# Performance work log

Hardware: AMD Instinct MI355X
Metric: run time of the kernel (lower is better)

Reference implementation:

```python
import jax, jax.numpy as jnp
import numpy as np

SEQ_LEN, BATCH, INPUT_SIZE, HIDDEN, OUTPUT_SIZE = 100, 2048, 128, 512, 128
DEC_STEPS = 29


def lstm_cell(x, h, c, W_ih, W_hh, b_ih, b_hh):
    # torch LSTMCell gate order: i, f, g, o
    gates = x @ W_ih.T + b_ih + h @ W_hh.T + b_hh
    i, f, g, o = jnp.split(gates, 4, axis=-1)
    i = jax.nn.sigmoid(i)
    f = jax.nn.sigmoid(f)
    g = jnp.tanh(g)
    o = jax.nn.sigmoid(o)
    c_new = f * c + i * g
    h_new = o * jnp.tanh(c_new)
    return h_new, c_new


def setup_inputs() -> dict:
    key = jax.random.key(0)
    ks = jax.random.split(key, 10)
    s = 0.05
    return {
        "input": jax.random.normal(ks[0], (SEQ_LEN, BATCH, INPUT_SIZE), jnp.float32),
        "hidden_encoder": jnp.zeros((BATCH, HIDDEN), jnp.float32),
        "hidden_decoder": jnp.zeros((BATCH, HIDDEN), jnp.float32),
        "cell_encoder": jnp.zeros((BATCH, HIDDEN), jnp.float32),
        "cell_decoder": jnp.zeros((BATCH, HIDDEN), jnp.float32),
        "W_ih_enc": jax.random.normal(ks[1], (4 * HIDDEN, INPUT_SIZE), jnp.float32) * s,
        "W_hh_enc": jax.random.normal(ks[2], (4 * HIDDEN, HIDDEN), jnp.float32) * s,
        "b_ih_enc": jax.random.normal(ks[3], (4 * HIDDEN,), jnp.float32) * s,
        "b_hh_enc": jax.random.normal(ks[4], (4 * HIDDEN,), jnp.float32) * s,
        "W_ih_dec": jax.random.normal(ks[5], (4 * HIDDEN, HIDDEN), jnp.float32) * s,
        "W_hh_dec": jax.random.normal(ks[6], (4 * HIDDEN, HIDDEN), jnp.float32) * s,
        "b_ih_dec": jax.random.normal(ks[7], (4 * HIDDEN,), jnp.float32) * s,
        "b_hh_dec": jax.random.normal(ks[8], (4 * HIDDEN,), jnp.float32) * s,
        "W_lin": jax.random.normal(ks[9], (OUTPUT_SIZE, HIDDEN), jnp.float32) * s,
        "b_lin": jnp.zeros((OUTPUT_SIZE,), jnp.float32),
    }


def reference(input, hidden_encoder, hidden_decoder, cell_encoder, cell_decoder,
              W_ih_enc, W_hh_enc, b_ih_enc, b_hh_enc,
              W_ih_dec, W_hh_dec, b_ih_dec, b_hh_dec, W_lin, b_lin):
    # Encoder: sequential LSTMCell over time
    def enc_step(carry, x_t):
        h, c = carry
        h, c = lstm_cell(x_t, h, c, W_ih_enc, W_hh_enc, b_ih_enc, b_hh_enc)
        return (h, c), None

    (h_enc, c_enc), _ = jax.lax.scan(enc_step, (hidden_encoder, cell_encoder), input)

    # Decoder: 29 steps; input to the cell IS the current hidden state
    def dec_step(carry, _):
        h, c = carry
        h, c = lstm_cell(h, h, c, W_ih_dec, W_hh_dec, b_ih_dec, b_hh_dec)
        return (h, c), h

    (h_dec, c_dec), dec_hs = jax.lax.scan(dec_step, (h_enc, cell_decoder), None, length=DEC_STEPS)

    hs = jnp.concatenate([h_enc[None], dec_hs], axis=0)  # [30, B, H]
    output = hs @ W_lin.T + b_lin                         # [30, B, output_size]
    return (output, h_enc, h_dec, c_enc, c_dec)
```

## Files before the change

### kernel.cpp

```cpp
#include <hip/hip_runtime.h>

#define B_   2048
#define H_   512
#define I_   128
#define G4   2048
#define SEQ  100
#define DEC  29
#define OUT_ 128
#define TEAM 16

typedef __attribute__((ext_vector_type(8))) short bf16x8;
typedef __attribute__((ext_vector_type(4))) float f32x4;
typedef __attribute__((address_space(3))) unsigned int       lds_u32;
typedef __attribute__((address_space(1))) const unsigned int glb_u32c;

__device__ inline unsigned short f2bf(float f) {
    union { float f; unsigned int u; } v; v.f = f;
    unsigned int u = v.u + 0x7fffu + ((v.u >> 16) & 1u);
    return (unsigned short)(u >> 16);
}
__device__ inline float sigm(float x)  { return 1.f / (1.f + __expf(-x)); }
__device__ inline float tanh_(float x) { return 2.f / (1.f + __expf(-2.f * x)) - 1.f; }

template <int AUX>
__device__ inline void gl16(const unsigned short* g, unsigned short* l) {
    __builtin_amdgcn_global_load_lds((glb_u32c*)g, (lds_u32*)l, 16, 0, AUX);
}

#define WAIT_VM(n) asm volatile("s_waitcnt vmcnt(" #n ")" ::: "memory")

template <int N> struct ic { static constexpr int v = N; };

__global__ __launch_bounds__(512, 2) void persist(
    const unsigned short* __restrict__ h0b,
    const unsigned short* __restrict__ xbf,
    const unsigned short* __restrict__ Wce,
    const unsigned short* __restrict__ Wd,
    const unsigned short* __restrict__ Wl,
    const float* __restrict__ be, const float* __restrict__ bd,
    const float* __restrict__ blin,
    const float* __restrict__ c_enc0, const float* __restrict__ c_dec0,
    unsigned short* __restrict__ hp0, unsigned short* __restrict__ hp1,
    unsigned short* __restrict__ hs,
    float* __restrict__ out_y,
    float* __restrict__ out_hEnc, float* __restrict__ out_cEnc,
    float* __restrict__ out_hDec, float* __restrict__ out_cDec,
    unsigned int* __restrict__ bar)
{
    __shared__ unsigned short smem[32768];

    const int tid  = threadIdx.x;
    const int b    = blockIdx.x;
    const int rg   = b & 15;
    const int cgB  = b >> 4;
    const int m0   = rg * 128;
    const int c0   = cgB * 32;

    const int lane = tid & 63, w = tid >> 6;
    const int quad = lane >> 4, l16 = lane & 15;
    const int bit3 = (lane >> 3) & 1;
    const int co   = lane & 7;
    const int wc   = w & 3;
    const int rbase = (w >> 2) * 64;
    const int jlo  = bit3 * 2;

    const int hcl  = wc * 8 + co;
    const int hcol = c0 + hcl;

    unsigned int* bcnt = bar + rg * 64;
    unsigned int* bgen = bcnt + 32;
    unsigned int  my_gen = 0;

    const int srow8 = lane >> 3;
    const int segl  = co ^ srow8;

    int lds_off[2];
#pragma unroll
    for (int ks = 0; ks < 2; ++ks)
        lds_off[ks] = (rbase + l16) * 128 + (((ks * 4 + quad) ^ (lane & 7)) * 16);

    bf16x8 Bw[2][20];
    f32x4  acc[4][2];
    float  c_reg[4][2];

    auto loadB = [&](const unsigned short* W, int Kw, int GS, int cb, int nks) {
#pragma unroll
        for (int cf = 0; cf < 2; ++cf) {
            const int grow = (cf * 2 + bit3) * GS + cb + hcl;
            const unsigned short* wp = W + (size_t)grow * Kw + quad * 8;
#pragma unroll
            for (int ksg = 0; ksg < 20; ++ksg)
                if (ksg < nks)
                    Bw[cf][ksg] = *(const bf16x8*)(wp + ksg * 32);
        }
    };

    auto gemm = [&](auto kcn_t, auto xt_t,
                    const unsigned short* Asrc, const unsigned short* xsrc) {
        constexpr int KCN = decltype(kcn_t)::v;
        constexpr int XT  = decltype(xt_t)::v;

        auto stg = [&](int kc, int buf, bool isx) {
            unsigned short* dstl = smem + buf * 8192 + w * 1024;
            if (isx) {
                const unsigned short* g0 =
                    xsrc + (m0 + w * 16 + srow8) * I_ + (kc - 8) * 64 + segl * 8;
                gl16<0>(g0, dstl);
                gl16<0>(g0 + 8 * I_, dstl + 512);
            } else {
                const unsigned short* g0 =
                    Asrc + (m0 + w * 16 + srow8) * H_ + kc * 64 + segl * 8;
                gl16<17>(g0, dstl);
                gl16<17>(g0 + 8 * H_, dstl + 512);
            }
        };

#pragma unroll
        for (int rf = 0; rf < 4; ++rf)
#pragma unroll
            for (int cf = 0; cf < 2; ++cf) acc[rf][cf] = (f32x4){0.f, 0.f, 0.f, 0.f};

        __syncthreads();
        stg(0, 0, false);
        stg(1, 1, false);
        stg(2, 2, false);
#pragma unroll
        for (int kc = 0; kc < KCN; ++kc) {
            if (kc < KCN - 2)      { WAIT_VM(4); }
            else if (kc == KCN - 2){ WAIT_VM(2); }
            else                   { WAIT_VM(0); }
            __builtin_amdgcn_s_barrier();
            __builtin_amdgcn_sched_barrier(0);
            if (kc + 3 < KCN) stg(kc + 3, (kc + 3) & 3, XT && (kc + 3) >= 8);

            const char* sb = (const char*)smem + ((kc & 3) * 16384);
            __builtin_amdgcn_s_setprio(1);
#pragma unroll
            for (int ks = 0; ks < 2; ++ks) {
                const int kk = kc * 2 + ks;
                const bf16x8 a0 = *(const bf16x8*)(sb + lds_off[ks]);
                const bf16x8 a1 = *(const bf16x8*)(sb + lds_off[ks] + 2048);
                const bf16x8 a2 = *(const bf16x8*)(sb + lds_off[ks] + 4096);
                const bf16x8 a3 = *(const bf16x8*)(sb + lds_off[ks] + 6144);
                acc[0][0] = __builtin_amdgcn_mfma_f32_16x16x32_bf16(a0, Bw[0][kk], acc[0][0], 0, 0, 0);
                acc[1][0] = __builtin_amdgcn_mfma_f32_16x16x32_bf16(a1, Bw[0][kk], acc[1][0], 0, 0, 0);
                acc[2][0] = __builtin_amdgcn_mfma_f32_16x16x32_bf16(a2, Bw[0][kk], acc[2][0], 0, 0, 0);
                acc[3][0] = __builtin_amdgcn_mfma_f32_16x16x32_bf16(a3, Bw[0][kk], acc[3][0], 0, 0, 0);
                acc[0][1] = __builtin_amdgcn_mfma_f32_16x16x32_bf16(a0, Bw[1][kk], acc[0][1], 0, 0, 0);
                acc[1][1] = __builtin_amdgcn_mfma_f32_16x16x32_bf16(a1, Bw[1][kk], acc[1][1], 0, 0, 0);
                acc[2][1] = __builtin_amdgcn_mfma_f32_16x16x32_bf16(a2, Bw[1][kk], acc[2][1], 0, 0, 0);
                acc[3][1] = __builtin_amdgcn_mfma_f32_16x16x32_bf16(a3, Bw[1][kk], acc[3][1], 0, 0, 0);
            }
            __builtin_amdgcn_s_setprio(0);
        }
    };

    auto team_barrier = [&]() {
        __syncthreads();
        if (tid == 0) {
            unsigned old = __hip_atomic_fetch_add(bcnt, 1u, __ATOMIC_RELAXED,
                                                  __HIP_MEMORY_SCOPE_AGENT);
            if (old == (my_gen + 1u) * TEAM - 1u) {
                __hip_atomic_fetch_add(bgen, 1u, __ATOMIC_RELAXED,
                                       __HIP_MEMORY_SCOPE_AGENT);
            } else {
                while (__hip_atomic_load(bgen, __ATOMIC_RELAXED,
                                         __HIP_MEMORY_SCOPE_AGENT) <= my_gen)
                    __builtin_amdgcn_s_sleep(2);
            }
        }
        my_gen++;
        __syncthreads();
    };

    auto cell_epi = [&](float bi, float bf_, float bg, float bo,
                        unsigned short* dst, float* hdump, float* cdump) {
        unsigned short* hstage = smem;
#pragma unroll
        for (int rf = 0; rf < 4; ++rf) {
#pragma unroll
            for (int jj = 0; jj < 2; ++jj) {
                const float a0lo = acc[rf][0][jj],     a0hi = acc[rf][0][2 + jj];
                const float a1lo = acc[rf][1][jj],     a1hi = acc[rf][1][2 + jj];
                const float p0lo = __shfl_xor(a0lo, 8), p0hi = __shfl_xor(a0hi, 8);
                const float p1lo = __shfl_xor(a1lo, 8), p1hi = __shfl_xor(a1hi, 8);
                const float own0 = bit3 ? a0hi : a0lo;
                const float own1 = bit3 ? a1hi : a1lo;
                const float par0 = bit3 ? p0hi : p0lo;
                const float par1 = bit3 ? p1hi : p1lo;
                const float gi = (bit3 ? par0 : own0) + bi;
                const float gf = (bit3 ? own0 : par0) + bf_;
                const float gg = (bit3 ? par1 : own1) + bg;
                const float go = (bit3 ? own1 : par1) + bo;
                const float ii = sigm(gi), ff = sigm(gf);
                const float g2 = tanh_(gg), oo = sigm(go);
                const float cn = ff * c_reg[rf][jj] + ii * g2;
                c_reg[rf][jj] = cn;
                const float hn = oo * tanh_(cn);
                const int row_l = rbase + rf * 16 + quad * 4 + jlo + jj;
                hstage[row_l * 32 + hcl] = f2bf(hn);
                if (hdump) {
                    const size_t idx = (size_t)(m0 + row_l) * H_ + hcol;
                    hdump[idx] = hn; cdump[idx] = cn;
                }
            }
        }
        __syncthreads();
        const unsigned int* h32 = (const unsigned int*)smem;
#pragma unroll
        for (int i = 0; i < 4; ++i) {
            const int idx = tid + i * 512;
            const int row = idx >> 4, cp = idx & 15;
            unsigned int* gp =
                (unsigned int*)(dst + (size_t)(m0 + row) * H_ + c0) + cp;
            __hip_atomic_store(gp, h32[idx], __ATOMIC_RELAXED,
                               __HIP_MEMORY_SCOPE_AGENT);
        }
    };

    {
        loadB(Wce, 640, H_, c0, 20);
        const float bi = be[hcol],            bf_ = be[H_ + hcol],
                    bg = be[2 * H_ + hcol],   bo  = be[3 * H_ + hcol];
#pragma unroll
        for (int rf = 0; rf < 4; ++rf)
#pragma unroll
            for (int jj = 0; jj < 2; ++jj) {
                const int row_l = rbase + rf * 16 + quad * 4 + jlo + jj;
                c_reg[rf][jj] = c_enc0[(size_t)(m0 + row_l) * H_ + hcol];
            }
        for (int t = 0; t < SEQ; ++t) {
            const unsigned short* src = (t == 0) ? h0b : ((t & 1) ? hp0 : hp1);
            unsigned short*       dst = (t == SEQ - 1) ? hs : ((t & 1) ? hp1 : hp0);
            const bool last = (t == SEQ - 1);
            gemm(ic<10>{}, ic<1>{}, src, xbf + (size_t)t * B_ * I_);
            cell_epi(bi, bf_, bg, bo, dst,
                     last ? out_hEnc : nullptr, last ? out_cEnc : nullptr);
            team_barrier();
        }
    }

    {
        loadB(Wd, 512, H_, c0, 16);
        const float bi = bd[hcol],            bf_ = bd[H_ + hcol],
                    bg = bd[2 * H_ + hcol],   bo  = bd[3 * H_ + hcol];
#pragma unroll
        for (int rf = 0; rf < 4; ++rf)
#pragma unroll
            for (int jj = 0; jj < 2; ++jj) {
                const int row_l = rbase + rf * 16 + quad * 4 + jlo + jj;
                c_reg[rf][jj] = c_dec0[(size_t)(m0 + row_l) * H_ + hcol];
            }
        for (int s = 0; s < DEC; ++s) {
            const bool last = (s == DEC - 1);
            gemm(ic<8>{}, ic<0>{}, hs + (size_t)s * B_ * H_, nullptr);
            cell_epi(bi, bf_, bg, bo, hs + (size_t)(s + 1) * B_ * H_,
                     last ? out_hDec : nullptr, last ? out_cDec : nullptr);
            team_barrier();
        }
    }

    {
        loadB(Wl, 512, 32, 0, 16);
        for (int s = cgB; s < DEC + 1; s += 16) {
            gemm(ic<8>{}, ic<0>{}, hs + (size_t)s * B_ * H_, nullptr);
#pragma unroll
            for (int cf = 0; cf < 2; ++cf) {
                const int oc = (cf * 2 + bit3) * 32 + hcl;
                const float bbv = blin[oc];
#pragma unroll
                for (int rf = 0; rf < 4; ++rf)
#pragma unroll
                    for (int j = 0; j < 4; ++j) {
                        const int row = m0 + rbase + rf * 16 + quad * 4 + j;
                        out_y[(size_t)s * B_ * OUT_ + (size_t)row * OUT_ + oc] =
                            acc[rf][cf][j] + bbv;
                    }
            }
        }
    }
}

__global__ void prep(const float* __restrict__ whh_e, const float* __restrict__ wih_e,
                     const float* __restrict__ wih_d, const float* __restrict__ whh_d,
                     const float* __restrict__ wlin,
                     const float* __restrict__ bie, const float* __restrict__ bhe,
                     const float* __restrict__ bid, const float* __restrict__ bhd,
                     unsigned short* __restrict__ Wce, unsigned short* __restrict__ Wd,
                     unsigned short* __restrict__ Wl,
                     float* __restrict__ be, float* __restrict__ bd)
{
    const int i = blockIdx.x * blockDim.x + threadIdx.x;
    if (i < G4 * 640) {
        const int r = i / 640, k = i % 640;
        Wce[i] = f2bf(k < H_ ? whh_e[r * H_ + k] : wih_e[r * I_ + (k - H_)]);
    }
    if (i < G4 * H_)   Wd[i] = f2bf(wih_d[i] + whh_d[i]);
    if (i < OUT_ * H_) Wl[i] = f2bf(wlin[i]);
    if (i < G4) { be[i] = bie[i] + bhe[i]; bd[i] = bid[i] + bhd[i]; }
}

__global__ void xconv(const float* __restrict__ x, unsigned short* __restrict__ xb, int n4)
{
    const int i = blockIdx.x * blockDim.x + threadIdx.x;
    if (i < n4) {
        const float4 f = *(const float4*)(x + (size_t)i * 4);
        ushort4 o;
        o.x = f2bf(f.x); o.y = f2bf(f.y); o.z = f2bf(f.z); o.w = f2bf(f.w);
        *(ushort4*)(xb + (size_t)i * 4) = o;
    }
}

__global__ void inith(const float* __restrict__ h0, unsigned short* __restrict__ hb)
{
    const int i = blockIdx.x * blockDim.x + threadIdx.x;
    if (i < B_ * H_) hb[i] = f2bf(h0[i]);
}

extern "C" void kernel_launch(void* const* d_in, const int* in_sizes, int n_in,
                              void* d_out, int out_size, void* d_ws, size_t ws_size,
                              hipStream_t stream) {
    (void)in_sizes; (void)n_in; (void)out_size; (void)ws_size;
    const float* input  = (const float*)d_in[0];
    const float* h_enc0 = (const float*)d_in[1];
    const float* c_enc0 = (const float*)d_in[3];
    const float* c_dec0 = (const float*)d_in[4];
    const float* Wih_e  = (const float*)d_in[5];
    const float* Whh_e  = (const float*)d_in[6];
    const float* bih_e  = (const float*)d_in[7];
    const float* bhh_e  = (const float*)d_in[8];
    const float* Wih_d  = (const float*)d_in[9];
    const float* Whh_d  = (const float*)d_in[10];
    const float* bih_d  = (const float*)d_in[11];
    const float* bhh_d  = (const float*)d_in[12];
    const float* Wlin   = (const float*)d_in[13];
    const float* blin   = (const float*)d_in[14];
    float* out = (float*)d_out;

    char* ws = (char*)d_ws;
    size_t off = 0;
    auto alloc = [&](size_t bytes) -> void* {
        void* p = ws + off;
        off = (off + bytes + 255) & ~(size_t)255;
        return p;
    };
    unsigned short* Wce = (unsigned short*)alloc((size_t)G4 * 640 * 2);
    unsigned short* Wd  = (unsigned short*)alloc((size_t)G4 * H_ * 2);
    unsigned short* Wl  = (unsigned short*)alloc((size_t)OUT_ * H_ * 2);
    float* be = (float*)alloc((size_t)G4 * 4);
    float* bd = (float*)alloc((size_t)G4 * 4);
    unsigned short* h0b = (unsigned short*)alloc((size_t)B_ * H_ * 2);
    unsigned short* hp0 = (unsigned short*)alloc((size_t)B_ * H_ * 2);
    unsigned short* hp1 = (unsigned short*)alloc((size_t)B_ * H_ * 2);
    unsigned short* xbf = (unsigned short*)alloc((size_t)SEQ * B_ * I_ * 2);
    unsigned short* hs  = (unsigned short*)alloc((size_t)(DEC + 1) * B_ * H_ * 2);
    unsigned int*   bar = (unsigned int*)alloc(16 * 64 * 4);

    float* out_y    = out;
    float* out_hEnc = out + (size_t)(DEC + 1) * B_ * OUT_;
    float* out_hDec = out_hEnc + (size_t)B_ * H_;
    float* out_cEnc = out_hDec + (size_t)B_ * H_;
    float* out_cDec = out_cEnc + (size_t)B_ * H_;

    prep<<<(G4 * 640 + 255) / 256, 256, 0, stream>>>(
        Whh_e, Wih_e, Wih_d, Whh_d, Wlin, bih_e, bhh_e, bih_d, bhh_d,
        Wce, Wd, Wl, be, bd);
    xconv<<<(SEQ * B_ * I_ / 4 + 255) / 256, 256, 0, stream>>>(input, xbf, SEQ * B_ * I_ / 4);
    inith<<<(B_ * H_ + 255) / 256, 256, 0, stream>>>(h_enc0, h0b);
    hipMemsetAsync(bar, 0, 16 * 64 * 4, stream);

    persist<<<256, 512, 0, stream>>>(
        h0b, xbf, Wce, Wd, Wl, be, bd, blin, c_enc0, c_dec0,
        hp0, hp1, hs, out_y, out_hEnc, out_cEnc, out_hDec, out_cDec, bar);
}
```

Before: 1.276 ms.

## Prefetch next-step x tile across team barrier and detect same-XCC teams

The encoder input tile for step t+1 is now staged into LDS before the inter-block team barrier, so the x part of the GEMM is moved off the recurrent critical path. The GEMM is reordered to consume the prefetched x chunks first. Each block reads its XCC id and checks whether all blocks in its team share it; if so, h loads use a different cache policy (gl16<1> instead of gl16<17>). The epilogue staging moves to a separate swizzled LDS region to avoid bank conflicts, and the team barrier uses raw s_barrier. This adds a startup handshake and depends on placement behaviour that is not guaranteed.

```diff
diff --git a/kernel.cpp b/kernel.cpp
--- a/kernel.cpp
+++ b/kernel.cpp
@@ -83,6 +83,48 @@
     f32x4  acc[4][2];
     float  c_reg[4][2];
 
+    unsigned int xcc;
+    asm volatile("s_getreg_b32 %0, hwreg(HW_REG_XCC_ID)" : "=s"(xcc));
+    xcc &= 15u;
+    unsigned int* xtab = bar + TEAM * 64;
+    if (tid == 0) {
+        __hip_atomic_store(xtab + b, xcc + 1u, __ATOMIC_RELAXED,
+                           __HIP_MEMORY_SCOPE_AGENT);
+        unsigned ok = 1;
+        for (int j = 0; j < TEAM; ++j) {
+            unsigned v = 0;
+            for (int spin = 0; spin < (1 << 20); ++spin) {
+                v = __hip_atomic_load(xtab + rg + 16 * j, __ATOMIC_RELAXED,
+                                      __HIP_MEMORY_SCOPE_AGENT);
+                if (v) break;
+                __builtin_amdgcn_s_sleep(8);
+            }
+            ok &= (v == xcc + 1u);
+        }
+        *(volatile unsigned int*)smem = ok;
+    }
+    __syncthreads();
+    const bool sx = (*(volatile unsigned int*)smem != 0);
+    __syncthreads();
+
+    auto stg_h = [&](const unsigned short* Asrc, int hk, int buf, bool sx_) {
+        unsigned short* dstl = smem + buf * 8192 + w * 1024;
+        const unsigned short* g0 =
+            Asrc + (size_t)(m0 + w * 16 + srow8) * H_ + hk * 64 + segl * 8;
+        if (sx_) { gl16<1>(g0, dstl);  gl16<1>(g0 + 8 * H_, dstl + 512); }
+        else     { gl16<17>(g0, dstl); gl16<17>(g0 + 8 * H_, dstl + 512); }
+    };
+    auto stg_x = [&](const unsigned short* xs) {
+#pragma unroll
+        for (int cx = 0; cx < 2; ++cx) {
+            unsigned short* dstl = smem + cx * 8192 + w * 1024;
+            const unsigned short* g0 =
+                xs + (size_t)(m0 + w * 16 + srow8) * I_ + cx * 64 + segl * 8;
+            gl16<0>(g0, dstl);
+            gl16<0>(g0 + 8 * I_, dstl + 512);
+        }
+    };
+
     auto loadB = [&](const unsigned short* W, int Kw, int GS, int cb, int nks) {
 #pragma unroll
         for (int cf = 0; cf < 2; ++cf) {
@@ -95,49 +137,32 @@
         }
     };
 
-    auto gemm = [&](auto kcn_t, auto xt_t,
-                    const unsigned short* Asrc, const unsigned short* xsrc) {
+    auto gemm = [&](auto kcn_t, auto pre_t, const unsigned short* Asrc, bool sx_) {
         constexpr int KCN = decltype(kcn_t)::v;
-        constexpr int XT  = decltype(xt_t)::v;
-
-        auto stg = [&](int kc, int buf, bool isx) {
-            unsigned short* dstl = smem + buf * 8192 + w * 1024;
-            if (isx) {
-                const unsigned short* g0 =
-                    xsrc + (m0 + w * 16 + srow8) * I_ + (kc - 8) * 64 + segl * 8;
-                gl16<0>(g0, dstl);
-                gl16<0>(g0 + 8 * I_, dstl + 512);
-            } else {
-                const unsigned short* g0 =
-                    Asrc + (m0 + w * 16 + srow8) * H_ + kc * 64 + segl * 8;
-                gl16<17>(g0, dstl);
-                gl16<17>(g0 + 8 * H_, dstl + 512);
-            }
-        };
-
+        constexpr int PRE = decltype(pre_t)::v;
 #pragma unroll
         for (int rf = 0; rf < 4; ++rf)
 #pragma unroll
             for (int cf = 0; cf < 2; ++cf) acc[rf][cf] = (f32x4){0.f, 0.f, 0.f, 0.f};
-
-        __syncthreads();
-        stg(0, 0, false);
-        stg(1, 1, false);
-        stg(2, 2, false);
+        if (PRE) { stg_h(Asrc, 0, 2, sx_); stg_h(Asrc, 1, 3, sx_); }
+        else     { stg_h(Asrc, 0, 0, sx_); stg_h(Asrc, 1, 1, sx_); stg_h(Asrc, 2, 2, sx_); }
 #pragma unroll
         for (int kc = 0; kc < KCN; ++kc) {
-            if (kc < KCN - 2)      { WAIT_VM(4); }
-            else if (kc == KCN - 2){ WAIT_VM(2); }
-            else                   { WAIT_VM(0); }
+            if (PRE && kc == 0)     { WAIT_VM(6); }
+            else if (kc < KCN - 2)  { WAIT_VM(4); }
+            else if (kc == KCN - 2) { WAIT_VM(2); }
+            else                    { WAIT_VM(0); }
             __builtin_amdgcn_s_barrier();
             __builtin_amdgcn_sched_barrier(0);
-            if (kc + 3 < KCN) stg(kc + 3, (kc + 3) & 3, XT && (kc + 3) >= 8);
+            if (kc + 3 < KCN && (!PRE || kc >= 1))
+                stg_h(Asrc, (PRE ? kc + 1 : kc + 3), (kc + 3) & 3, sx_);
 
             const char* sb = (const char*)smem + ((kc & 3) * 16384);
+            const int kb = PRE ? (kc < 2 ? 16 + kc * 2 : (kc - 2) * 2) : kc * 2;
             __builtin_amdgcn_s_setprio(1);
 #pragma unroll
             for (int ks = 0; ks < 2; ++ks) {
-                const int kk = kc * 2 + ks;
+                const int kk = kb + ks;
                 const bf16x8 a0 = *(const bf16x8*)(sb + lds_off[ks]);
                 const bf16x8 a1 = *(const bf16x8*)(sb + lds_off[ks] + 2048);
                 const bf16x8 a2 = *(const bf16x8*)(sb + lds_off[ks] + 4096);
@@ -155,8 +180,9 @@
         }
     };
 
-    auto team_barrier = [&]() {
-        __syncthreads();
+    auto team_sync = [&]() {
+        __builtin_amdgcn_sched_barrier(0);
+        __builtin_amdgcn_s_barrier();
         if (tid == 0) {
             unsigned old = __hip_atomic_fetch_add(bcnt, 1u, __ATOMIC_RELAXED,
                                                   __HIP_MEMORY_SCOPE_AGENT);
@@ -170,18 +196,19 @@
             }
         }
         my_gen++;
-        __syncthreads();
+        __builtin_amdgcn_s_barrier();
+        __builtin_amdgcn_sched_barrier(0);
     };
 
     auto cell_epi = [&](float bi, float bf_, float bg, float bo,
                         unsigned short* dst, float* hdump, float* cdump) {
-        unsigned short* hstage = smem;
+        unsigned short* hstage = smem + 16384;
 #pragma unroll
         for (int rf = 0; rf < 4; ++rf) {
 #pragma unroll
             for (int jj = 0; jj < 2; ++jj) {
-                const float a0lo = acc[rf][0][jj],     a0hi = acc[rf][0][2 + jj];
-                const float a1lo = acc[rf][1][jj],     a1hi = acc[rf][1][2 + jj];
+                const float a0lo = acc[rf][0][jj],      a0hi = acc[rf][0][2 + jj];
+                const float a1lo = acc[rf][1][jj],      a1hi = acc[rf][1][2 + jj];
                 const float p0lo = __shfl_xor(a0lo, 8), p0hi = __shfl_xor(a0hi, 8);
                 const float p1lo = __shfl_xor(a1lo, 8), p1hi = __shfl_xor(a1hi, 8);
                 const float own0 = bit3 ? a0hi : a0lo;
@@ -198,7 +225,8 @@
                 c_reg[rf][jj] = cn;
                 const float hn = oo * tanh_(cn);
                 const int row_l = rbase + rf * 16 + quad * 4 + jlo + jj;
-                hstage[row_l * 32 + hcl] = f2bf(hn);
+                const int scol  = hcl ^ (((row_l & 2) << 3) | ((row_l & 4) << 1));
+                hstage[row_l * 32 + scol] = f2bf(hn);
                 if (hdump) {
                     const size_t idx = (size_t)(m0 + row_l) * H_ + hcol;
                     hdump[idx] = hn; cdump[idx] = cn;
@@ -206,17 +234,21 @@
             }
         }
         __syncthreads();
-        const unsigned int* h32 = (const unsigned int*)smem;
+        const unsigned int* h32 = (const unsigned int*)(smem + 16384);
 #pragma unroll
         for (int i = 0; i < 4; ++i) {
             const int idx = tid + i * 512;
             const int row = idx >> 4, cp = idx & 15;
+            const int cps = cp ^ (((row & 2) << 2) | (row & 4));
+            const unsigned int val = h32[row * 16 + cps];
             unsigned int* gp =
                 (unsigned int*)(dst + (size_t)(m0 + row) * H_ + c0) + cp;
-            __hip_atomic_store(gp, h32[idx], __ATOMIC_RELAXED,
+            __hip_atomic_store(gp, val, __ATOMIC_RELAXED,
                                __HIP_MEMORY_SCOPE_AGENT);
         }
     };
+
+    stg_x(xbf);
 
     {
         loadB(Wce, 640, H_, c0, 20);
@@ -233,10 +265,12 @@
             const unsigned short* src = (t == 0) ? h0b : ((t & 1) ? hp0 : hp1);
             unsigned short*       dst = (t == SEQ - 1) ? hs : ((t & 1) ? hp1 : hp0);
             const bool last = (t == SEQ - 1);
-            gemm(ic<10>{}, ic<1>{}, src, xbf + (size_t)t * B_ * I_);
+            gemm(ic<10>{}, ic<1>{}, src, sx);
             cell_epi(bi, bf_, bg, bo, dst,
                      last ? out_hEnc : nullptr, last ? out_cEnc : nullptr);
-            team_barrier();
+            WAIT_VM(0);
+            if (t + 1 < SEQ) stg_x(xbf + (size_t)(t + 1) * B_ * I_);
+            team_sync();
         }
     }
 
@@ -253,17 +287,18 @@
             }
         for (int s = 0; s < DEC; ++s) {
             const bool last = (s == DEC - 1);
-            gemm(ic<8>{}, ic<0>{}, hs + (size_t)s * B_ * H_, nullptr);
+            gemm(ic<8>{}, ic<0>{}, hs + (size_t)s * B_ * H_, sx);
             cell_epi(bi, bf_, bg, bo, hs + (size_t)(s + 1) * B_ * H_,
                      last ? out_hDec : nullptr, last ? out_cDec : nullptr);
-            team_barrier();
+            WAIT_VM(0);
+            team_sync();
         }
     }
 
     {
         loadB(Wl, 512, 32, 0, 16);
         for (int s = cgB; s < DEC + 1; s += 16) {
-            gemm(ic<8>{}, ic<0>{}, hs + (size_t)s * B_ * H_, nullptr);
+            gemm(ic<8>{}, ic<0>{}, hs + (size_t)s * B_ * H_, sx);
 #pragma unroll
             for (int cf = 0; cf < 2; ++cf) {
                 const int oc = (cf * 2 + bit3) * 32 + hcl;
@@ -354,7 +389,7 @@
     unsigned short* hp1 = (unsigned short*)alloc((size_t)B_ * H_ * 2);
     unsigned short* xbf = (unsigned short*)alloc((size_t)SEQ * B_ * I_ * 2);
     unsigned short* hs  = (unsigned short*)alloc((size_t)(DEC + 1) * B_ * H_ * 2);
-    unsigned int*   bar = (unsigned int*)alloc(16 * 64 * 4);
+    unsigned int*   bar = (unsigned int*)alloc((16 * 64 + 256) * 4);
 
     float* out_y    = out;
     float* out_hEnc = out + (size_t)(DEC + 1) * B_ * OUT_;
@@ -367,7 +402,7 @@
         Wce, Wd, Wl, be, bd);
     xconv<<<(SEQ * B_ * I_ / 4 + 255) / 256, 256, 0, stream>>>(input, xbf, SEQ * B_ * I_ / 4);
     inith<<<(B_ * H_ + 255) / 256, 256, 0, stream>>>(h_enc0, h0b);
-    hipMemsetAsync(bar, 0, 16 * 64 * 4, stream);
+    hipMemsetAsync(bar, 0, (16 * 64 + 256) * 4, stream);
 
     persist<<<256, 512, 0, stream>>>(
         h0b, xbf, Wce, Wd, Wl, be, bd, blin, c_enc0, c_dec0,
```

Measured after the change: 1.669 ms. +30.9%, slower.
